# Performance work log

Hardware: AMD Instinct MI355X
Metric: run time of the kernel (lower is better)

The kernel has to match this reference:

```python
import jax, jax.numpy as jnp
import numpy as np

DIM = 768
NUM_HEADS = 16
HEAD_DIM = DIM // NUM_HEADS        # 48
AXIS_DIM = HEAD_DIM // 3           # 16 dims per spatial axis (t, y, x)
ROPE_BASE = 10000.0
T, H, W = 8, 14, 14                # N = 1568


def setup_inputs() -> dict:
    key = jax.random.key(0)
    k1, k2, k3 = jax.random.split(key, 3)
    B, N = 4, T * H * W
    x = jax.random.normal(k1, (B, N, DIM), dtype=jnp.float32)
    # 3D position grid (t, y, x) for each token
    t, y, xg = np.meshgrid(np.arange(T), np.arange(H), np.arange(W), indexing="ij")
    pos = jnp.asarray(np.stack([t.ravel(), y.ravel(), xg.ravel()], axis=-1), dtype=jnp.int32)  # [N,3]
    W_qkv = jax.random.normal(k2, (DIM, 3 * DIM), dtype=jnp.float32) * (DIM ** -0.5)
    W_proj = jax.random.normal(k3, (DIM, DIM), dtype=jnp.float32) * (DIM ** -0.5)
    b_proj = jnp.zeros((DIM,), dtype=jnp.float32)
    return {"x": x, "pos": pos, "W_qkv": W_qkv, "W_proj": W_proj, "b_proj": b_proj}


def _rope3d(q, k, pos):
    # q, k: [B, H, N, HEAD_DIM]; pos: [N, 3] int
    half = AXIS_DIM // 2  # 8 frequency pairs per axis
    inv_freq = ROPE_BASE ** (-jnp.arange(half, dtype=jnp.float32) / half)  # [half]
    # angles per axis: [N, 3, half]
    ang = pos.astype(jnp.float32)[:, :, None] * inv_freq[None, None, :]
    cos = jnp.cos(ang)  # [N, 3, half]
    sin = jnp.sin(ang)

    def rotate(t):
        # split head_dim into 3 axis chunks of AXIS_DIM, rotate_half within each
        t3 = t.reshape(*t.shape[:-1], 3, AXIS_DIM)          # [B,H,N,3,AXIS_DIM]
        t1, t2 = t3[..., :half], t3[..., half:]             # [B,H,N,3,half]
        c = cos[None, None]                                  # [1,1,N,3,half]
        s = sin[None, None]
        r = jnp.concatenate([t1 * c - t2 * s, t2 * c + t1 * s], axis=-1)
        return r.reshape(*t.shape)

    return rotate(q), rotate(k)


def reference(x, pos, W_qkv, W_proj, b_proj):
    B, N, C = x.shape
    scale = 1.0 / jnp.sqrt(jnp.asarray(HEAD_DIM, dtype=x.dtype))
    qkv = (x @ W_qkv).reshape(B, N, 3, NUM_HEADS, HEAD_DIM)
    qkv = jnp.transpose(qkv, (2, 0, 3, 1, 4))               # [3,B,H,N,Dh]
    q, k, v = qkv[0], qkv[1], qkv[2]
    q, k = _rope3d(q, k, pos)
    attn = jnp.einsum("bhnd,bhmd->bhnm", q, k) * scale      # [B,H,N,N]
    attn = jax.nn.softmax(attn, axis=-1)
    out = jnp.einsum("bhnm,bhmd->bhnd", attn, v)            # [B,H,N,Dh]
    out = jnp.transpose(out, (0, 2, 1, 3)).reshape(B, N, C)
    return out @ W_proj + b_proj
```

## Files before the change

### kernel.cpp

```cpp
#include <hip/hip_runtime.h>
#include <hip/hip_bf16.h>
#include <math.h>

#define DIM 768
#define NHEADS 16
#define HD 48
#define NTOK 1568
#define BATCH 4
#define ROWS (BATCH * NTOK)
#define QKV_COLS (3 * DIM)

typedef __attribute__((ext_vector_type(8))) _Float16 f16x8;
typedef __attribute__((ext_vector_type(2))) __fp16 fp16v2;
typedef __attribute__((ext_vector_type(4))) float f32x4;

__device__ inline ushort f2h(float f) {
    union { _Float16 h; ushort u; } v; v.h = (_Float16)f; return v.u;
}
__device__ inline float h2f(ushort u) {
    union { _Float16 h; ushort u; } v; v.u = u; return (float)v.h;
}

__device__ inline void gl16(const void* g, void* l) {
    __builtin_amdgcn_global_load_lds(
        (const __attribute__((address_space(1))) unsigned int*)g,
        (__attribute__((address_space(3))) unsigned int*)l, 16, 0, 0);
}

__global__ void cast_f32_f16(const float* __restrict__ in, ushort* __restrict__ out, int n4) {
    int i = blockIdx.x * blockDim.x + threadIdx.x;
    if (i >= n4) return;
    float4 v = ((const float4*)in)[i];
    ushort4 o;
    o.x = f2h(v.x); o.y = f2h(v.y); o.z = f2h(v.z); o.w = f2h(v.w);
    ((ushort4*)out)[i] = o;
}

__global__ void transpose_cast(const float* __restrict__ in, ushort* __restrict__ out,
                               int R, int C) {
    __shared__ ushort tile[32][33];
    int tx = threadIdx.x, ty = threadIdx.y;
    int c0 = blockIdx.x * 32, r0 = blockIdx.y * 32;
#pragma unroll
    for (int k = 0; k < 4; ++k)
        tile[ty + 8 * k][tx] = f2h(in[(size_t)(r0 + ty + 8 * k) * C + c0 + tx]);
    __syncthreads();
#pragma unroll
    for (int k = 0; k < 4; ++k)
        out[(size_t)(c0 + ty + 8 * k) * R + r0 + tx] = tile[tx][ty + 8 * k];
}

#define GBK 64

template <int BM>
__global__ __launch_bounds__(256) void gemm_f16(
    const ushort* __restrict__ A, const ushort* __restrict__ Bt,
    float* __restrict__ Cf, ushort* __restrict__ Cb, ushort* __restrict__ Vt,
    const float* __restrict__ bias, const int* __restrict__ pos,
    int M, int N, int K) {
    constexpr int MI = BM / 32;
    __shared__ ushort sA[2][BM * 64];
    __shared__ ushort sB[2][128 * 64];
    const int tid = threadIdx.x;
    const int wid = tid >> 6, lane = tid & 63;
    const int wm = wid >> 1, wn = wid & 1;
    const int m0 = blockIdx.y * BM, n0 = blockIdx.x * 128;
    const int lr = lane & 15, g = lane >> 4;

    auto STAGE = [&](int buf, int k0) {
#pragma unroll
        for (int i = 0; i < MI; ++i) {
            int c = tid + 256 * i;
            int row = c >> 3;
            int ch = (c & 7) ^ (row & 7);
            gl16(&A[(size_t)(m0 + row) * K + k0 + ch * 8], &sA[buf][(c & ~63) * 8]);
        }
#pragma unroll
        for (int i = 0; i < 4; ++i) {
            int c = tid + 256 * i;
            int row = c >> 3;
            int ch = (c & 7) ^ (row & 7);
            gl16(&Bt[(size_t)(n0 + row) * K + k0 + ch * 8], &sB[buf][(c & ~63) * 8]);
        }
    };

    f32x4 acc[MI][4] = {};
    const int NK = K / GBK;
    STAGE(0, 0);
    for (int t = 0; t < NK; ++t) {
        const int cur = t & 1;
        asm volatile("s_waitcnt vmcnt(0)" ::: "memory");
        __builtin_amdgcn_s_barrier();
        if (t + 1 < NK) STAGE(cur ^ 1, (t + 1) * GBK);
#pragma unroll
        for (int k2 = 0; k2 < GBK; k2 += 32) {
            f16x8 af[MI], bg[4];
#pragma unroll
            for (int f = 0; f < MI; ++f) {
                int ra = wm * (BM / 2) + f * 16 + lr;
                int ba = (ra * 128 + k2 * 2 + g * 16) ^ ((ra & 7) << 4);
                af[f] = *(const f16x8*)((const char*)sA[cur] + ba);
            }
#pragma unroll
            for (int f = 0; f < 4; ++f) {
                int rb = wn * 64 + f * 16 + lr;
                int bb = (rb * 128 + k2 * 2 + g * 16) ^ ((rb & 7) << 4);
                bg[f] = *(const f16x8*)((const char*)sB[cur] + bb);
            }
#pragma unroll
            for (int mi = 0; mi < MI; ++mi)
#pragma unroll
                for (int ni = 0; ni < 4; ++ni)
                    acc[mi][ni] = __builtin_amdgcn_mfma_f32_16x16x32_f16(
                        bg[ni], af[mi], acc[mi][ni], 0, 0, 0);
        }
    }
    const bool vpath = (Vt != nullptr) && (n0 >= 2 * DIM);
    const float RINV = 0.31622776601683794f;
    const float RINV4 = 0.01f;
#pragma unroll
    for (int mi = 0; mi < MI; ++mi) {
        int m = m0 + wm * (BM / 2) + mi * 16 + lr;
#pragma unroll
        for (int ni = 0; ni < 4; ++ni) {
            int nb = n0 + wn * 64 + ni * 16 + g * 4;
            if (Cf) {
                float4 b4 = *(const float4*)&bias[nb];
                float4 o4;
                o4.x = acc[mi][ni][0] + b4.x;
                o4.y = acc[mi][ni][1] + b4.y;
                o4.z = acc[mi][ni][2] + b4.z;
                o4.w = acc[mi][ni][3] + b4.w;
                *(float4*)&Cf[(size_t)m * N + nb] = o4;
            } else if (vpath) {
                int bb = m / NTOK, tok = m % NTOK;
#pragma unroll
                for (int j = 0; j < 4; ++j)
                    Vt[((size_t)bb * DIM + (nb - 2 * DIM + j)) * NTOK + tok] =
                        f2h(acc[mi][ni][j]);
            } else {
                float vv[4];
#pragma unroll
                for (int j = 0; j < 4; ++j) vv[j] = acc[mi][ni][j];
                if (pos) {
                    int tok = m % NTOK;
                    int axis = (nb >> 4) % 3;
                    float p = (float)pos[tok * 3 + axis];
                    float fj = (g & 1) ? RINV4 : 1.0f;
                    bool hi = (g & 2) != 0;
#pragma unroll
                    for (int j = 0; j < 4; ++j) {
                        float s, c; __sincosf(p * fj, &s, &c); fj *= RINV;
                        float part = __shfl_xor(vv[j], 32);
                        vv[j] = hi ? (vv[j] * c + part * s) : (vv[j] * c - part * s);
                    }
                }
                union { fp16v2 h; uint u; } c0, c1;
                c0.h = __builtin_amdgcn_cvt_pkrtz(vv[0], vv[1]);
                c1.h = __builtin_amdgcn_cvt_pkrtz(vv[2], vv[3]);
                uint2 uu; uu.x = c0.u; uu.y = c1.u;
                *(uint2*)&Cb[(size_t)m * N + nb] = uu;
            }
        }
    }
}

#define QBLK 128
#define KVB 32
#define NT (NTOK / KVB)
#define PP 40

__global__ __launch_bounds__(256) void attn_mfma(const ushort* __restrict__ qkv,
                                                 const ushort* __restrict__ vt,
                                                 ushort* __restrict__ aout) {
    __shared__ ushort sK3[3][KVB * 64];
    __shared__ ushort sV3[3][64 * 32];
    __shared__ ushort sP[4][32 * PP];
    const int tid = threadIdx.x, w = tid >> 6, lane = tid & 63;
    const int b = blockIdx.x >> 4, h = blockIdx.x & 15;
    const int q0 = blockIdx.y * QBLK;
    const size_t bbase = (size_t)b * NTOK * QKV_COLS;
    const size_t vbase = ((size_t)b * DIM + h * HD) * NTOK;
    const int lr = lane & 15, g = lane >> 4, lk = g << 3;
    const float qs = 0.14433756729740643f * 1.4426950408889634f;
    const float M2 = 14.0f;

    if (tid < 32) {
        sV3[0][48 * 32 + tid] = 0x3C00;
        sV3[1][48 * 32 + tid] = 0x3C00;
        sV3[2][48 * 32 + tid] = 0x3C00;
    }
    asm volatile("s_waitcnt lgkmcnt(0)" ::: "memory");

    f16x8 aq[2][2];
#pragma unroll
    for (int rb = 0; rb < 2; ++rb) {
        int qr = q0 + w * 32 + rb * 16 + lr;
        if (qr >= NTOK) qr = NTOK - 1;
        const ushort* qp = &qkv[bbase + (size_t)qr * QKV_COLS + h * HD];
        ushort r0[8], r1[8];
        *(ushort4*)&r0[0] = *(const ushort4*)&qp[lk];
        *(ushort4*)&r0[4] = *(const ushort4*)&qp[lk + 4];
        if (g < 2) {
            *(ushort4*)&r1[0] = *(const ushort4*)&qp[32 + lk];
            *(ushort4*)&r1[4] = *(const ushort4*)&qp[32 + lk + 4];
        } else {
#pragma unroll
            for (int e = 0; e < 8; ++e) r1[e] = 0;
        }
        f16x8 a0, a1;
#pragma unroll
        for (int e = 0; e < 8; ++e) {
            a0[e] = (_Float16)(h2f(r0[e]) * qs);
            a1[e] = (_Float16)(h2f(r1[e]) * qs);
        }
        aq[rb][0] = a0; aq[rb][1] = a1;
    }

    auto STAGE = [&](int buf, int kv0) {
        {
            int c = tid, row = c >> 3;
            int ch = (c & 7) ^ (row & 7);
            gl16(&qkv[bbase + (size_t)(kv0 + row) * QKV_COLS + DIM + h * HD + ch * 8],
                 &sK3[buf][(c & ~63) * 8]);
        }
        if (lane < 48) {
            int c = w * 48 + lane, d = c >> 2;
            int cc = (c & 3) ^ ((d >> 1) & 3);
            gl16(&vt[vbase + (size_t)d * NTOK + kv0 + cc * 8],
                 &sV3[buf][w * 384]);
        }
    };

    f32x4 o[2][4] = {};

    STAGE(0, 0);
    STAGE(1, KVB);
    for (int t = 0; t < NT; ++t) {
        const int cur = t % 3;
        if (t + 1 < NT) asm volatile("s_waitcnt vmcnt(2)" ::: "memory");
        else            asm volatile("s_waitcnt vmcnt(0)" ::: "memory");
        __builtin_amdgcn_s_barrier();
        if (t + 2 < NT) STAGE((t + 2) % 3, (t + 2) * KVB);

        f16x8 bk[2][2];
#pragma unroll
        for (int f = 0; f < 2; ++f)
#pragma unroll
            for (int ks = 0; ks < 2; ++ks) {
                int row = f * 16 + lr;
                int byt = (row * 128 + ks * 64 + g * 16) ^ ((lr & 7) << 4);
                bk[f][ks] = *(const f16x8*)((const char*)sK3[cur] + byt);
            }
        f32x4 sacc[2][2] = {{{-M2, -M2, -M2, -M2}, {-M2, -M2, -M2, -M2}},
                            {{-M2, -M2, -M2, -M2}, {-M2, -M2, -M2, -M2}}};
        __builtin_amdgcn_s_setprio(1);
#pragma unroll
        for (int rb = 0; rb < 2; ++rb)
#pragma unroll
            for (int f = 0; f < 2; ++f) {
                sacc[rb][f] = __builtin_amdgcn_mfma_f32_16x16x32_f16(bk[f][0], aq[rb][0], sacc[rb][f], 0, 0, 0);
                sacc[rb][f] = __builtin_amdgcn_mfma_f32_16x16x32_f16(bk[f][1], aq[rb][1], sacc[rb][f], 0, 0, 0);
            }
        __builtin_amdgcn_s_setprio(0);

#pragma unroll
        for (int rb = 0; rb < 2; ++rb)
#pragma unroll
            for (int f = 0; f < 2; ++f) {
                float p[4];
#pragma unroll
                for (int j = 0; j < 4; ++j) {
                    float pv;
                    asm("v_exp_f32 %0, %1" : "=v"(pv) : "v"(sacc[rb][f][j]));
                    p[j] = pv;
                }
                union { fp16v2 h; uint u; } c0, c1;
                c0.h = __builtin_amdgcn_cvt_pkrtz(p[0], p[1]);
                c1.h = __builtin_amdgcn_cvt_pkrtz(p[2], p[3]);
                uint2 uu; uu.x = c0.u; uu.y = c1.u;
                *(uint2*)&sP[w][(rb * 16 + lr) * PP + f * 16 + 4 * g] = uu;
            }

        f16x8 bv[4];
#pragma unroll
        for (int nf = 0; nf < 4; ++nf) {
            int row = nf * 16 + lr;
            int byt = (row * 64 + g * 16) ^ (((lr >> 1) & 3) << 4);
            bv[nf] = *(const f16x8*)((const char*)sV3[cur] + byt);
        }
        __builtin_amdgcn_s_setprio(1);
#pragma unroll
        for (int rb = 0; rb < 2; ++rb) {
            f16x8 pa = *(const f16x8*)&sP[w][(rb * 16 + lr) * PP + lk];
#pragma unroll
            for (int nf = 0; nf < 4; ++nf)
                o[rb][nf] = __builtin_amdgcn_mfma_f32_16x16x32_f16(bv[nf], pa, o[rb][nf], 0, 0, 0);
        }
        __builtin_amdgcn_s_setprio(0);
    }

#pragma unroll
    for (int rb = 0; rb < 2; ++rb) {
        float lv = __shfl(o[rb][3][0], lr, 64);
        int qr = q0 + w * 32 + rb * 16 + lr;
        if (qr < NTOK) {
            float inv = 1.f / lv;
            size_t rbse = ((size_t)b * NTOK + qr) * DIM;
#pragma unroll
            for (int nf = 0; nf < 3; ++nf) {
                ushort4 h4;
#pragma unroll
                for (int j = 0; j < 4; ++j)
                    ((ushort*)&h4)[j] = f2h(o[rb][nf][j] * inv);
                *(ushort4*)&aout[rbse + h * HD + nf * 16 + 4 * g] = h4;
            }
        }
    }
}

extern "C" void kernel_launch(void* const* d_in, const int* in_sizes, int n_in,
                              void* d_out, int out_size, void* d_ws, size_t ws_size,
                              hipStream_t stream) {
    const float* x   = (const float*)d_in[0];
    const int*   pos = (const int*)d_in[1];
    const float* Wq  = (const float*)d_in[2];
    const float* Wp  = (const float*)d_in[3];
    const float* bp  = (const float*)d_in[4];
    float* out = (float*)d_out;

    ushort* ws     = (ushort*)d_ws;
    ushort* x_h    = ws;
    ushort* WqT    = x_h + (size_t)ROWS * DIM;
    ushort* WpT    = WqT + (size_t)QKV_COLS * DIM;
    ushort* qkv_h  = WpT + (size_t)DIM * DIM;
    ushort* aout   = qkv_h + (size_t)ROWS * QKV_COLS;
    ushort* vt     = aout + (size_t)ROWS * DIM;

    cast_f32_f16<<<(ROWS * DIM / 4 + 255) / 256, 256, 0, stream>>>(x, x_h, ROWS * DIM / 4);
    transpose_cast<<<dim3(QKV_COLS / 32, DIM / 32), dim3(32, 8), 0, stream>>>(Wq, WqT, DIM, QKV_COLS);
    transpose_cast<<<dim3(DIM / 32, DIM / 32), dim3(32, 8), 0, stream>>>(Wp, WpT, DIM, DIM);

    gemm_f16<128><<<dim3(QKV_COLS / 128, ROWS / 128), 256, 0, stream>>>(
        x_h, WqT, nullptr, qkv_h, vt, nullptr, pos, ROWS, QKV_COLS, DIM);

    attn_mfma<<<dim3(BATCH * NHEADS, (NTOK + QBLK - 1) / QBLK), 256, 0, stream>>>(qkv_h, vt, aout);

    gemm_f16<64><<<dim3(DIM / 128, ROWS / 64), 256, 0, stream>>>(
        aout, WpT, out, nullptr, nullptr, bp, nullptr, ROWS, DIM, DIM);
}
```

Baseline: 142.9 us.

## Double KV tile to 64 with double buffering and a masked tail tile

The attention kernel now processes 64 keys per iteration instead of 32. It switches from a triple-buffered to a double-buffered LDS ring, with a new swizzle layout for K and V. The final tile, which is half past the end of the sequence, is handled by zeroing the P entries beyond NTOK. This halves the number of barriers and loop iterations and gives more MFMA work per LDS stage. In exchange, the prefetch depth drops to one tile with a full vmcnt(0) wait, and the tail tile loads K/V rows past the sequence end, which may read out of bounds for the last batch/head.

Measured after the change: 151.2 us. +5.8%, slower.

```diff
diff --git a/kernel.cpp b/kernel.cpp
--- a/kernel.cpp
+++ b/kernel.cpp
@@ -166,15 +166,15 @@
 }
 
 #define QBLK 128
-#define KVB 32
-#define NT (NTOK / KVB)
-#define PP 40
+#define KVB 64
+#define NT ((NTOK + KVB - 1) / KVB)
+#define PP 72
 
 __global__ __launch_bounds__(256) void attn_mfma(const ushort* __restrict__ qkv,
                                                  const ushort* __restrict__ vt,
                                                  ushort* __restrict__ aout) {
-    __shared__ ushort sK3[3][KVB * 64];
-    __shared__ ushort sV3[3][64 * 32];
+    __shared__ ushort sK2[2][KVB * 64];
+    __shared__ ushort sV2[2][64 * 64];
     __shared__ ushort sP[4][32 * PP];
     const int tid = threadIdx.x, w = tid >> 6, lane = tid & 63;
     const int b = blockIdx.x >> 4, h = blockIdx.x & 15;
@@ -185,10 +185,9 @@
     const float qs = 0.14433756729740643f * 1.4426950408889634f;
     const float M2 = 14.0f;
 
-    if (tid < 32) {
-        sV3[0][48 * 32 + tid] = 0x3C00;
-        sV3[1][48 * 32 + tid] = 0x3C00;
-        sV3[2][48 * 32 + tid] = 0x3C00;
+    if (tid < 64) {
+        sV2[0][48 * 64 + tid] = 0x3C00;
+        sV2[1][48 * 64 + tid] = 0x3C00;
     }
     asm volatile("s_waitcnt lgkmcnt(0)" ::: "memory");
 
@@ -219,83 +218,96 @@
 
     auto STAGE = [&](int buf, int kv0) {
         {
-            int c = tid, row = c >> 3;
-            int ch = (c & 7) ^ (row & 7);
+            int c = tid, row = c >> 3, ch = (c & 7) ^ (row & 7);
             gl16(&qkv[bbase + (size_t)(kv0 + row) * QKV_COLS + DIM + h * HD + ch * 8],
-                 &sK3[buf][(c & ~63) * 8]);
-        }
-        if (lane < 48) {
-            int c = w * 48 + lane, d = c >> 2;
-            int cc = (c & 3) ^ ((d >> 1) & 3);
+                 &sK2[buf][(w * 64) * 8]);
+            int c2 = 256 + tid, row2 = c2 >> 3, ch2 = (c2 & 7) ^ (row2 & 7);
+            gl16(&qkv[bbase + (size_t)(kv0 + row2) * QKV_COLS + DIM + h * HD + ch2 * 8],
+                 &sK2[buf][(256 + w * 64) * 8]);
+        }
+        {
+            int c = tid, d = c >> 3, cc = (c & 7) ^ (d & 7);
             gl16(&vt[vbase + (size_t)d * NTOK + kv0 + cc * 8],
-                 &sV3[buf][w * 384]);
+                 &sV2[buf][(w * 64) * 8]);
+            if (lane < 32) {
+                int c2 = 256 + w * 32 + lane, d2 = c2 >> 3, cc2 = (c2 & 7) ^ (d2 & 7);
+                gl16(&vt[vbase + (size_t)d2 * NTOK + kv0 + cc2 * 8],
+                     &sV2[buf][(256 + w * 32) * 8]);
+            }
         }
     };
 
     f32x4 o[2][4] = {};
 
     STAGE(0, 0);
-    STAGE(1, KVB);
     for (int t = 0; t < NT; ++t) {
-        const int cur = t % 3;
-        if (t + 1 < NT) asm volatile("s_waitcnt vmcnt(2)" ::: "memory");
-        else            asm volatile("s_waitcnt vmcnt(0)" ::: "memory");
+        const int cur = t & 1;
+        const bool tail = (t == NT - 1);
+        asm volatile("s_waitcnt vmcnt(0)" ::: "memory");
         __builtin_amdgcn_s_barrier();
-        if (t + 2 < NT) STAGE((t + 2) % 3, (t + 2) * KVB);
-
-        f16x8 bk[2][2];
-#pragma unroll
-        for (int f = 0; f < 2; ++f)
-#pragma unroll
-            for (int ks = 0; ks < 2; ++ks) {
-                int row = f * 16 + lr;
-                int byt = (row * 128 + ks * 64 + g * 16) ^ ((lr & 7) << 4);
-                bk[f][ks] = *(const f16x8*)((const char*)sK3[cur] + byt);
-            }
-        f32x4 sacc[2][2] = {{{-M2, -M2, -M2, -M2}, {-M2, -M2, -M2, -M2}},
-                            {{-M2, -M2, -M2, -M2}, {-M2, -M2, -M2, -M2}}};
+        if (t + 1 < NT) STAGE(cur ^ 1, (t + 1) * KVB);
+
+        f32x4 sacc[2][4];
+#pragma unroll
+        for (int rb = 0; rb < 2; ++rb)
+#pragma unroll
+            for (int f = 0; f < 4; ++f) {
+                f32x4 c = {-M2, -M2, -M2, -M2};
+                sacc[rb][f] = c;
+            }
         __builtin_amdgcn_s_setprio(1);
 #pragma unroll
+        for (int f = 0; f < 4; ++f) {
+            int row = f * 16 + lr;
+            int b0 = (row * 128 + g * 16) ^ ((row & 7) << 4);
+            int b1 = (row * 128 + 64 + g * 16) ^ ((row & 7) << 4);
+            f16x8 bk0 = *(const f16x8*)((const char*)sK2[cur] + b0);
+            f16x8 bk1 = *(const f16x8*)((const char*)sK2[cur] + b1);
+            sacc[0][f] = __builtin_amdgcn_mfma_f32_16x16x32_f16(bk0, aq[0][0], sacc[0][f], 0, 0, 0);
+            sacc[0][f] = __builtin_amdgcn_mfma_f32_16x16x32_f16(bk1, aq[0][1], sacc[0][f], 0, 0, 0);
+            sacc[1][f] = __builtin_amdgcn_mfma_f32_16x16x32_f16(bk0, aq[1][0], sacc[1][f], 0, 0, 0);
+            sacc[1][f] = __builtin_amdgcn_mfma_f32_16x16x32_f16(bk1, aq[1][1], sacc[1][f], 0, 0, 0);
+        }
+        __builtin_amdgcn_s_setprio(0);
+
+#pragma unroll
         for (int rb = 0; rb < 2; ++rb)
 #pragma unroll
-            for (int f = 0; f < 2; ++f) {
-                sacc[rb][f] = __builtin_amdgcn_mfma_f32_16x16x32_f16(bk[f][0], aq[rb][0], sacc[rb][f], 0, 0, 0);
-                sacc[rb][f] = __builtin_amdgcn_mfma_f32_16x16x32_f16(bk[f][1], aq[rb][1], sacc[rb][f], 0, 0, 0);
-            }
-        __builtin_amdgcn_s_setprio(0);
-
-#pragma unroll
-        for (int rb = 0; rb < 2; ++rb)
-#pragma unroll
-            for (int f = 0; f < 2; ++f) {
-                float p[4];
-#pragma unroll
-                for (int j = 0; j < 4; ++j) {
-                    float pv;
-                    asm("v_exp_f32 %0, %1" : "=v"(pv) : "v"(sacc[rb][f][j]));
-                    p[j] = pv;
+            for (int f = 0; f < 4; ++f) {
+                uint2 uu;
+                if (tail && f >= 2) {
+                    uu.x = 0; uu.y = 0;
+                } else {
+                    float p[4];
+#pragma unroll
+                    for (int j = 0; j < 4; ++j) {
+                        float pv;
+                        asm("v_exp_f32 %0, %1" : "=v"(pv) : "v"(sacc[rb][f][j]));
+                        p[j] = pv;
+                    }
+                    union { fp16v2 h; uint u; } c0, c1;
+                    c0.h = __builtin_amdgcn_cvt_pkrtz(p[0], p[1]);
+                    c1.h = __builtin_amdgcn_cvt_pkrtz(p[2], p[3]);
+                    uu.x = c0.u; uu.y = c1.u;
                 }
-                union { fp16v2 h; uint u; } c0, c1;
-                c0.h = __builtin_amdgcn_cvt_pkrtz(p[0], p[1]);
-                c1.h = __builtin_amdgcn_cvt_pkrtz(p[2], p[3]);
-                uint2 uu; uu.x = c0.u; uu.y = c1.u;
                 *(uint2*)&sP[w][(rb * 16 + lr) * PP + f * 16 + 4 * g] = uu;
             }
 
-        f16x8 bv[4];
-#pragma unroll
-        for (int nf = 0; nf < 4; ++nf) {
-            int row = nf * 16 + lr;
-            int byt = (row * 64 + g * 16) ^ (((lr >> 1) & 3) << 4);
-            bv[nf] = *(const f16x8*)((const char*)sV3[cur] + byt);
-        }
         __builtin_amdgcn_s_setprio(1);
 #pragma unroll
         for (int rb = 0; rb < 2; ++rb) {
-            f16x8 pa = *(const f16x8*)&sP[w][(rb * 16 + lr) * PP + lk];
-#pragma unroll
-            for (int nf = 0; nf < 4; ++nf)
-                o[rb][nf] = __builtin_amdgcn_mfma_f32_16x16x32_f16(bv[nf], pa, o[rb][nf], 0, 0, 0);
+            f16x8 pa0 = *(const f16x8*)&sP[w][(rb * 16 + lr) * PP + lk];
+            f16x8 pa1 = *(const f16x8*)&sP[w][(rb * 16 + lr) * PP + 32 + lk];
+#pragma unroll
+            for (int nf = 0; nf < 4; ++nf) {
+                int row = nf * 16 + lr;
+                int b0 = (row * 128 + g * 16) ^ ((row & 7) << 4);
+                int b1 = (row * 128 + 64 + g * 16) ^ ((row & 7) << 4);
+                f16x8 bv0 = *(const f16x8*)((const char*)sV2[cur] + b0);
+                f16x8 bv1 = *(const f16x8*)((const char*)sV2[cur] + b1);
+                o[rb][nf] = __builtin_amdgcn_mfma_f32_16x16x32_f16(bv0, pa0, o[rb][nf], 0, 0, 0);
+                o[rb][nf] = __builtin_amdgcn_mfma_f32_16x16x32_f16(bv1, pa1, o[rb][nf], 0, 0, 0);
+            }
         }
         __builtin_amdgcn_s_setprio(0);
     }
```

## Split attention over KV range into two partitions with combine kernel

Applied to the files above, without the earlier changes.

Adds a split-KV (flash-decoding style) partition: the attention grid gets a z dimension of 2, with each half processing a subset of the KV tiles and writing unnormalized fp16 outputs plus row sums. A new combine kernel adds the partials and normalizes. The goal is more blocks for better CU occupancy (64x13 grid was under-filling the GPU). This relies on the fixed softmax max offset being shared so the partials can simply be summed, and it costs extra global traffic, fp16 rounding of unnormalized partials, and one additional launch.

After: 149.1 us. 4.3% more time.

```diff
diff --git a/kernel.cpp b/kernel.cpp
--- a/kernel.cpp
+++ b/kernel.cpp
@@ -168,17 +168,22 @@
 #define QBLK 128
 #define KVB 32
 #define NT (NTOK / KVB)
+#define TSPLIT 25
 #define PP 40
 
 __global__ __launch_bounds__(256) void attn_mfma(const ushort* __restrict__ qkv,
                                                  const ushort* __restrict__ vt,
-                                                 ushort* __restrict__ aout) {
+                                                 ushort* __restrict__ op0,
+                                                 ushort* __restrict__ op1,
+                                                 float* __restrict__ lpart) {
     __shared__ ushort sK3[3][KVB * 64];
     __shared__ ushort sV3[3][64 * 32];
     __shared__ ushort sP[4][32 * PP];
     const int tid = threadIdx.x, w = tid >> 6, lane = tid & 63;
     const int b = blockIdx.x >> 4, h = blockIdx.x & 15;
     const int q0 = blockIdx.y * QBLK;
+    const int z = blockIdx.z;
+    const int t0 = z ? TSPLIT : 0, t1 = z ? NT : TSPLIT;
     const size_t bbase = (size_t)b * NTOK * QKV_COLS;
     const size_t vbase = ((size_t)b * DIM + h * HD) * NTOK;
     const int lr = lane & 15, g = lane >> 4, lk = g << 3;
@@ -234,14 +239,14 @@
 
     f32x4 o[2][4] = {};
 
-    STAGE(0, 0);
-    STAGE(1, KVB);
-    for (int t = 0; t < NT; ++t) {
+    STAGE(t0 % 3, t0 * KVB);
+    STAGE((t0 + 1) % 3, (t0 + 1) * KVB);
+    for (int t = t0; t < t1; ++t) {
         const int cur = t % 3;
-        if (t + 1 < NT) asm volatile("s_waitcnt vmcnt(2)" ::: "memory");
+        if (t + 1 < t1) asm volatile("s_waitcnt vmcnt(2)" ::: "memory");
         else            asm volatile("s_waitcnt vmcnt(0)" ::: "memory");
         __builtin_amdgcn_s_barrier();
-        if (t + 2 < NT) STAGE((t + 2) % 3, (t + 2) * KVB);
+        if (t + 2 < t1) STAGE((t + 2) % 3, (t + 2) * KVB);
 
         f16x8 bk[2][2];
 #pragma unroll
@@ -300,22 +305,48 @@
         __builtin_amdgcn_s_setprio(0);
     }
 
+    ushort* op = z ? op1 : op0;
 #pragma unroll
     for (int rb = 0; rb < 2; ++rb) {
-        float lv = __shfl(o[rb][3][0], lr, 64);
         int qr = q0 + w * 32 + rb * 16 + lr;
         if (qr < NTOK) {
-            float inv = 1.f / lv;
+            if (g == 0)
+                lpart[((size_t)z * BATCH * NHEADS + b * NHEADS + h) * NTOK + qr] = o[rb][3][0];
             size_t rbse = ((size_t)b * NTOK + qr) * DIM;
 #pragma unroll
             for (int nf = 0; nf < 3; ++nf) {
                 ushort4 h4;
 #pragma unroll
                 for (int j = 0; j < 4; ++j)
-                    ((ushort*)&h4)[j] = f2h(o[rb][nf][j] * inv);
-                *(ushort4*)&aout[rbse + h * HD + nf * 16 + 4 * g] = h4;
-            }
-        }
+                    ((ushort*)&h4)[j] = f2h(o[rb][nf][j]);
+                *(ushort4*)&op[rbse + h * HD + nf * 16 + 4 * g] = h4;
+            }
+        }
+    }
+}
+
+__global__ void attn_combine(const ushort* __restrict__ op0,
+                             const ushort* __restrict__ op1,
+                             const float* __restrict__ lpart,
+                             ushort* __restrict__ aout) {
+    int idx = blockIdx.x * blockDim.x + threadIdx.x;
+    if (idx >= ROWS * NHEADS) return;
+    int row = idx >> 4, h = idx & 15;
+    int b = row / NTOK, q = row % NTOK;
+    size_t li = ((size_t)b * NHEADS + h) * NTOK + q;
+    float l = lpart[li] + lpart[(size_t)BATCH * NHEADS * NTOK + li];
+    float inv = 1.0f / l;
+    size_t base = (size_t)row * DIM + h * HD;
+#pragma unroll
+    for (int c = 0; c < 12; ++c) {
+        ushort4 a = *(const ushort4*)&op0[base + c * 4];
+        ushort4 bb = *(const ushort4*)&op1[base + c * 4];
+        ushort4 r;
+        ((ushort*)&r)[0] = f2h((h2f(a.x) + h2f(bb.x)) * inv);
+        ((ushort*)&r)[1] = f2h((h2f(a.y) + h2f(bb.y)) * inv);
+        ((ushort*)&r)[2] = f2h((h2f(a.z) + h2f(bb.z)) * inv);
+        ((ushort*)&r)[3] = f2h((h2f(a.w) + h2f(bb.w)) * inv);
+        *(ushort4*)&aout[base + c * 4] = r;
     }
 }
 
@@ -336,6 +367,9 @@
     ushort* qkv_h  = WpT + (size_t)DIM * DIM;
     ushort* aout   = qkv_h + (size_t)ROWS * QKV_COLS;
     ushort* vt     = aout + (size_t)ROWS * DIM;
+    ushort* op1    = vt + (size_t)ROWS * DIM;
+    float*  lpart  = (float*)(op1 + (size_t)ROWS * DIM);
+    ushort* op0    = x_h;
 
     cast_f32_f16<<<(ROWS * DIM / 4 + 255) / 256, 256, 0, stream>>>(x, x_h, ROWS * DIM / 4);
     transpose_cast<<<dim3(QKV_COLS / 32, DIM / 32), dim3(32, 8), 0, stream>>>(Wq, WqT, DIM, QKV_COLS);
@@ -344,7 +378,10 @@
     gemm_f16<128><<<dim3(QKV_COLS / 128, ROWS / 128), 256, 0, stream>>>(
         x_h, WqT, nullptr, qkv_h, vt, nullptr, pos, ROWS, QKV_COLS, DIM);
 
-    attn_mfma<<<dim3(BATCH * NHEADS, (NTOK + QBLK - 1) / QBLK), 256, 0, stream>>>(qkv_h, vt, aout);
+    attn_mfma<<<dim3(BATCH * NHEADS, (NTOK + QBLK - 1) / QBLK, 2), 256, 0, stream>>>(
+        qkv_h, vt, op0, op1, lpart);
+
+    attn_combine<<<(ROWS * NHEADS + 255) / 256, 256, 0, stream>>>(op0, op1, lpart, aout);
 
     gemm_f16<64><<<dim3(DIM / 128, ROWS / 64), 256, 0, stream>>>(
         aout, WpT, out, nullptr, nullptr, bp, nullptr, ROWS, DIM, DIM);
```
